# Performance work log

Measured on AMD Instinct MI355X. Metric: run time of the kernel, lower is better.

Reference implementation:

```python
import jax, jax.numpy as jnp
import numpy as np

MARGIN = 0.3
MIN_POS_DIST = 0.1
PUSH_SCALE = 2.0
DISSIMILAR_REL = 1  # dissimilar_relation_ids == {1}


def setup_inputs() -> dict:
    key = jax.random.key(0)
    k1, k2, k3, k4, k5 = jax.random.split(key, 5)
    B, D = 16384, 1024
    h = jax.random.normal(k1, (B, D), dtype=jnp.float32)
    t = jax.random.normal(k2, (B, D), dtype=jnp.float32)
    r = jax.random.normal(k3, (B, D), dtype=jnp.float32)
    relation_ids = jax.random.randint(k4, (B,), 0, 10, dtype=jnp.int64 if jax.config.jax_enable_x64 else jnp.int32)
    neg = jax.random.randint(k5, (B,), 0, B, dtype=relation_ids.dtype)
    idx = jnp.arange(B, dtype=neg.dtype)
    neg_idx = jnp.where(neg == idx, (neg + 1) % B, neg)  # enforce neg_idx[i] != i
    return {"h": h, "t": t, "r": r, "relation_ids": relation_ids, "neg_idx": neg_idx}


def reference(h, t, r, relation_ids, neg_idx):
    # pos_dist[i] = ||h[i] + r[i] - t[i]||_2
    hr = h + r                                  # [B, D]
    pos_dist = jnp.linalg.norm(hr - t, axis=-1)  # [B]
    # neg_dist[i] = ||h[i] + r[i] - t[neg_idx[i]]||_2
    neg_dist = jnp.linalg.norm(hr - t[neg_idx], axis=-1)  # [B]

    dissim = relation_ids == DISSIMILAR_REL
    curr_margin = MARGIN * PUSH_SCALE
    loss_dissim = jax.nn.relu(curr_margin - pos_dist) + 0.5 * jnp.exp(-pos_dist)
    loss_sim = jax.nn.relu(pos_dist - neg_dist + MARGIN) + 0.3 * jax.nn.relu(MIN_POS_DIST - pos_dist)
    per_sample = jnp.where(dissim, loss_dissim, loss_sim)
    return jnp.mean(per_sample)
```

## Files before the change

kernel.cpp:

```cpp
#include <hip/hip_runtime.h>
#include <math.h>


#define BDIM 16384
#define DDIM 1024

typedef float vfloat4 __attribute__((ext_vector_type(4)));

__global__ void zero_out_kernel(float* __restrict__ out) { out[0] = 0.0f; }

__global__ __launch_bounds__(256) void triplet_fused_kernel(
    const float* __restrict__ h, const float* __restrict__ t,
    const float* __restrict__ r, const int* __restrict__ rel,
    const int* __restrict__ neg, float* __restrict__ out)
{
    const int wave = threadIdx.x >> 6;
    const int lane = threadIdx.x & 63;
    const int row  = (blockIdx.x << 2) + wave;

    const int nidx = neg[row];
    const int rl   = rel[row];

    const vfloat4* h4 = (const vfloat4*)(h + (size_t)row * DDIM);
    const vfloat4* r4 = (const vfloat4*)(r + (size_t)row * DDIM);
    const vfloat4* t4 = (const vfloat4*)(t + (size_t)row * DDIM);
    const vfloat4* n4 = (rl == 1) ? t4 : (const vfloat4*)(t + (size_t)nidx * DDIM);

    float psum = 0.0f, nsum = 0.0f;
#pragma unroll
    for (int j = 0; j < 4; ++j) {
        const int k = lane + (j << 6);
        vfloat4 hv = __builtin_nontemporal_load(&h4[k]);
        vfloat4 rv = __builtin_nontemporal_load(&r4[k]);
        vfloat4 tv = t4[k];
        vfloat4 nv = n4[k];

        vfloat4 a = hv + rv;
        vfloat4 d = a - tv;
        psum += d.x * d.x + d.y * d.y + d.z * d.z + d.w * d.w;
        vfloat4 e = a - nv;
        nsum += e.x * e.x + e.y * e.y + e.z * e.z + e.w * e.w;
    }

#pragma unroll
    for (int off = 32; off > 0; off >>= 1) {
        psum += __shfl_down(psum, off, 64);
        nsum += __shfl_down(nsum, off, 64);
    }

    __shared__ float sm[4];
    if (lane == 0) {
        float pos = sqrtf(psum);
        float negd = sqrtf(nsum);
        float loss;
        if (rl == 1) loss = fmaxf(0.6f - pos, 0.0f) + 0.5f * expf(-pos);
        else         loss = fmaxf(pos - negd + 0.3f, 0.0f)
                          + 0.3f * fmaxf(0.1f - pos, 0.0f);
        sm[wave] = loss;
    }
    __syncthreads();
    if (threadIdx.x == 0) {
        float blk = (sm[0] + sm[1] + sm[2] + sm[3]) * (1.0f / (float)BDIM);
        atomicAdd(out, blk);
    }
}

extern "C" void kernel_launch(void* const* d_in, const int* in_sizes, int n_in,
                              void* d_out, int out_size, void* d_ws, size_t ws_size,
                              hipStream_t stream) {
    const float* h = (const float*)d_in[0];
    const float* t = (const float*)d_in[1];
    const float* r = (const float*)d_in[2];
    const int* rel = (const int*)d_in[3];
    const int* neg = (const int*)d_in[4];
    float* out = (float*)d_out;

    zero_out_kernel<<<1, 1, 0, stream>>>(out);
    triplet_fused_kernel<<<BDIM / 4, 256, 0, stream>>>(h, t, r, rel, neg, out);
}
```

Measured before the change: 208.5 us.

## Stage row loads through LDS with double-buffered async global_load_lds

Replaces direct vector global loads with global_load_lds into a per-wave double-buffered LDS region, using explicit vmcnt waits to overlap the next chunk's loads with the current chunk's math. The aim is to hide memory latency with an explicit software pipeline. It uses 32 KB of LDS per block, which may reduce occupancy, and allows only two chunks in flight, fewer than the fully unrolled direct loads had.

```diff
diff --git a/kernel.cpp b/kernel.cpp
--- a/kernel.cpp
+++ b/kernel.cpp
@@ -7,13 +7,24 @@
 
 typedef float vfloat4 __attribute__((ext_vector_type(4)));
 
+#define GLD_LDS(gsrc, ldst)                                                  \
+    __builtin_amdgcn_global_load_lds(                                        \
+        (const __attribute__((address_space(1))) void*)(gsrc),               \
+        (__attribute__((address_space(3))) void*)(ldst), 16, 0, 0)
+
+#define WAITCNT_VM4 0x0F74
+#define WAITCNT_VM0 0x0F70
+
 __global__ void zero_out_kernel(float* __restrict__ out) { out[0] = 0.0f; }
 
-__global__ __launch_bounds__(256) void triplet_fused_kernel(
+__global__ __launch_bounds__(256) void triplet_lds_kernel(
     const float* __restrict__ h, const float* __restrict__ t,
     const float* __restrict__ r, const int* __restrict__ rel,
     const int* __restrict__ neg, float* __restrict__ out)
 {
+    __shared__ __align__(16) char smem[4 * 8192];
+    __shared__ float sm[4];
+
     const int wave = threadIdx.x >> 6;
     const int lane = threadIdx.x & 63;
     const int row  = (blockIdx.x << 2) + wave;
@@ -21,24 +32,43 @@
     const int nidx = neg[row];
     const int rl   = rel[row];
 
-    const vfloat4* h4 = (const vfloat4*)(h + (size_t)row * DDIM);
-    const vfloat4* r4 = (const vfloat4*)(r + (size_t)row * DDIM);
-    const vfloat4* t4 = (const vfloat4*)(t + (size_t)row * DDIM);
-    const vfloat4* n4 = (rl == 1) ? t4 : (const vfloat4*)(t + (size_t)nidx * DDIM);
+    const float* hb = h + (size_t)row * DDIM;
+    const float* rb = r + (size_t)row * DDIM;
+    const float* tb = t + (size_t)row * DDIM;
+    const float* nb = (rl == 1) ? tb : t + (size_t)nidx * DDIM;
 
+    char* base = smem + (wave << 13);
+
+    auto issue = [&](int c, int b) {
+        const int go = (c << 8) + (lane << 2);
+        char* lb = base + (b << 12);
+        GLD_LDS(hb + go, lb);
+        GLD_LDS(rb + go, lb + 1024);
+        GLD_LDS(tb + go, lb + 2048);
+        GLD_LDS(nb + go, lb + 3072);
+    };
+
+    issue(0, 0);
     float psum = 0.0f, nsum = 0.0f;
 #pragma unroll
-    for (int j = 0; j < 4; ++j) {
-        const int k = lane + (j << 6);
-        vfloat4 hv = __builtin_nontemporal_load(&h4[k]);
-        vfloat4 rv = __builtin_nontemporal_load(&r4[k]);
-        vfloat4 tv = t4[k];
-        vfloat4 nv = n4[k];
-
+    for (int c = 0; c < 4; ++c) {
+        if (c < 3) {
+            issue(c + 1, (c + 1) & 1);
+            __builtin_amdgcn_s_waitcnt(WAITCNT_VM4);
+        } else {
+            __builtin_amdgcn_s_waitcnt(WAITCNT_VM0);
+        }
+        __builtin_amdgcn_sched_barrier(0);
+        const char* lb = base + ((c & 1) << 12);
+        const int lo = lane << 4;
+        vfloat4 hv = *(const vfloat4*)(lb + lo);
+        vfloat4 rv = *(const vfloat4*)(lb + 1024 + lo);
+        vfloat4 tv = *(const vfloat4*)(lb + 2048 + lo);
+        vfloat4 nv = *(const vfloat4*)(lb + 3072 + lo);
         vfloat4 a = hv + rv;
         vfloat4 d = a - tv;
+        vfloat4 e = a - nv;
         psum += d.x * d.x + d.y * d.y + d.z * d.z + d.w * d.w;
-        vfloat4 e = a - nv;
         nsum += e.x * e.x + e.y * e.y + e.z * e.z + e.w * e.w;
     }
 
@@ -48,7 +78,6 @@
         nsum += __shfl_down(nsum, off, 64);
     }
 
-    __shared__ float sm[4];
     if (lane == 0) {
         float pos = sqrtf(psum);
         float negd = sqrtf(nsum);
@@ -76,5 +105,5 @@
     float* out = (float*)d_out;
 
     zero_out_kernel<<<1, 1, 0, stream>>>(out);
-    triplet_fused_kernel<<<BDIM / 4, 256, 0, stream>>>(h, t, r, rel, neg, out);
+    triplet_lds_kernel<<<BDIM / 4, 256, 0, stream>>>(h, t, r, rel, neg, out);
 }
```

Result: no change. 205.7 us (-1.3%).
